# Performance work log

Measured on AMD Instinct MI355X. Metric: run time of the kernel, lower is better.

Reference implementation:

```python
import jax, jax.numpy as jnp
import numpy as np

BINS = 256          # bins_per_sample (== embedding_dim, required by the module's math)
NUM_EMB = 256       # num_embeddings
EMB_DIM = 256       # embedding_dim
# dropout_prob = 0.1 -> identity in eval mode (reference runs deterministic/eval)


def setup_inputs() -> dict:
    key = jax.random.key(0)
    k1, k2 = jax.random.split(key)
    sequence_embeddings = jax.random.normal(k1, (2, 4, BINS, EMB_DIM), dtype=jnp.float32)
    emb_table = jax.random.normal(k2, (NUM_EMB, EMB_DIM), dtype=jnp.float32)
    return {"sequence_embeddings": sequence_embeddings, "emb_table": emb_table}


def reference(sequence_embeddings, emb_table):
    # relative-distance index: |i - j| clamped to [0, NUM_EMB-1]  -> [bins, bins]
    idx = jnp.arange(BINS)
    dist_idx = jnp.clip(jnp.abs(idx[:, None] - idx[None, :]), 0, NUM_EMB - 1)
    dist_embed = emb_table[dist_idx]                      # [bins, bins, d]

    # x1[..., i, j, d] = x[..., j, d];  x2[..., i, j, d] = x[..., i, d]
    x1 = sequence_embeddings[..., None, :, :]             # [..., 1,    bins, d]
    x2 = sequence_embeddings[..., :, None, :]             # [..., bins, 1,    d]

    # (x1 + x2)/2 + x1*x2 + distance embedding (dropout = identity in eval)
    return (x1 + x2) * 0.5 + x1 * x2 + dist_embed
```

## Files before the change

kernel.cpp:

```cpp
#include <hip/hip_runtime.h>

#define BINS 256
#define EMBV 64
#define BH   8

typedef float f32x4 __attribute__((ext_vector_type(4)));

__global__ __launch_bounds__(512) void outputhead_sym(
        const f32x4* __restrict__ seq4,
        const f32x4* __restrict__ tab4,
        f32x4* __restrict__ out4)
{
    const int blk = blockIdx.x;
    const int bh  = blk >> 7;
    const int b   = blk & 127;
    const int t   = threadIdx.x;
    const int d4  = t & 63;
    const int tj  = t >> 6;

    const size_t seq_base = (size_t)bh * BINS * EMBV;
    const size_t out_bh   = (size_t)bh * BINS * BINS * EMBV;

    #pragma unroll
    for (int r = 0; r < 2; ++r) {
        const int i = (r == 0) ? b : (BINS - 1 - b);
        const f32x4 si = seq4[seq_base + (size_t)i * EMBV + d4];
        const size_t out_row_i = out_bh + (size_t)i * BINS * EMBV;

        for (int jb = 0; jb <= i; jb += 8) {
            const int j = jb + tj;
            if (j > i) break;

            const f32x4 sj = seq4[seq_base + (size_t)j * EMBV + d4];
            const f32x4 tv = tab4[(size_t)(i - j) * EMBV + d4];

            const f32x4 o = (si + sj) * 0.5f + si * sj + tv;

            __builtin_nontemporal_store(o, &out4[out_row_i + (size_t)j * EMBV + d4]);
            if (j != i) {
                __builtin_nontemporal_store(
                    o, &out4[out_bh + (size_t)j * BINS * EMBV + (size_t)i * EMBV + d4]);
            }
        }
    }
}

extern "C" void kernel_launch(void* const* d_in, const int* in_sizes, int n_in,
                              void* d_out, int out_size, void* d_ws, size_t ws_size,
                              hipStream_t stream) {
    const f32x4* seq4 = (const f32x4*)d_in[0];
    const f32x4* tab4 = (const f32x4*)d_in[1];
    f32x4* out4 = (f32x4*)d_out;

    dim3 grid(BH * 128);
    dim3 block(512);
    outputhead_sym<<<grid, block, 0, stream>>>(seq4, tab4, out4);
}
```

Measured before the change: 114.6 us.

## Replace symmetric dual-store scheme with one block per output row

The kernel no longer computes the lower triangle and mirrors each result into the transposed position. Each block now owns one output row (i, bh) and writes it contiguously with ordinary stores, computing |i-j| directly. This removes the strided transposed stores and the uneven triangular work per block, at the cost of recomputing the symmetric half and dropping the nontemporal store hints. Block size and grid mapping change as well, interleaving bh in block order.

```diff
diff --git a/kernel.cpp b/kernel.cpp
--- a/kernel.cpp
+++ b/kernel.cpp
@@ -6,42 +6,34 @@
 
 typedef float f32x4 __attribute__((ext_vector_type(4)));
 
-__global__ __launch_bounds__(512) void outputhead_sym(
+__global__ __launch_bounds__(256) void outputhead_kernel(
         const f32x4* __restrict__ seq4,
         const f32x4* __restrict__ tab4,
         f32x4* __restrict__ out4)
 {
     const int blk = blockIdx.x;
-    const int bh  = blk >> 7;
-    const int b   = blk & 127;
+    const int bh  = blk & 7;
+    const int i   = blk >> 3;
     const int t   = threadIdx.x;
     const int d4  = t & 63;
     const int tj  = t >> 6;
 
-    const size_t seq_base = (size_t)bh * BINS * EMBV;
-    const size_t out_bh   = (size_t)bh * BINS * BINS * EMBV;
+    const f32x4 si = seq4[(bh * BINS + i) * EMBV + d4];
 
-    #pragma unroll
-    for (int r = 0; r < 2; ++r) {
-        const int i = (r == 0) ? b : (BINS - 1 - b);
-        const f32x4 si = seq4[seq_base + (size_t)i * EMBV + d4];
-        const size_t out_row_i = out_bh + (size_t)i * BINS * EMBV;
+    const size_t seq_bh_base  = (size_t)bh * BINS * EMBV;
+    const size_t out_row_base = ((size_t)(bh * BINS + i)) * BINS * EMBV;
 
-        for (int jb = 0; jb <= i; jb += 8) {
-            const int j = jb + tj;
-            if (j > i) break;
+    #pragma unroll 4
+    for (int jb = 0; jb < BINS; jb += 4) {
+        const int j    = jb + tj;
+        const int dist = (i > j) ? (i - j) : (j - i);
 
-            const f32x4 sj = seq4[seq_base + (size_t)j * EMBV + d4];
-            const f32x4 tv = tab4[(size_t)(i - j) * EMBV + d4];
+        const f32x4 sj = seq4[seq_bh_base + (size_t)j * EMBV + d4];
+        const f32x4 tv = tab4[(size_t)dist * EMBV + d4];
 
-            const f32x4 o = (si + sj) * 0.5f + si * sj + tv;
+        const f32x4 o = (si + sj) * 0.5f + si * sj + tv;
 
-            __builtin_nontemporal_store(o, &out4[out_row_i + (size_t)j * EMBV + d4]);
-            if (j != i) {
-                __builtin_nontemporal_store(
-                    o, &out4[out_bh + (size_t)j * BINS * EMBV + (size_t)i * EMBV + d4]);
-            }
-        }
+        out4[out_row_base + (size_t)j * EMBV + d4] = o;
     }
 }
 
@@ -52,7 +44,7 @@
     const f32x4* tab4 = (const f32x4*)d_in[1];
     f32x4* out4 = (f32x4*)d_out;
 
-    dim3 grid(BH * 128);
-    dim3 block(512);
-    outputhead_sym<<<grid, block, 0, stream>>>(seq4, tab4, out4);
+    dim3 grid(BH * BINS);
+    dim3 block(256);
+    outputhead_kernel<<<grid, block, 0, stream>>>(seq4, tab4, out4);
 }
```

New measurement: 98.21 us. -14.3%, faster.
